# Kernel tuning notes

Hardware: AMD Instinct MI355X
Metric: run time of the kernel (lower is better)

The kernel has to match this reference:

```python
import jax, jax.numpy as jnp
import numpy as np

B, N, L, D, H, NLAYERS, V = 8, 1024, 16, 256, 4, 2, 32000
DH = D // H  # per-head dim


def setup_inputs() -> dict:
    key = jax.random.key(0)
    ks = jax.random.split(key, 7)
    cfg_adj = jax.random.randint(ks[0], (B, N, N), 0, 2, dtype=jnp.int32)
    cfg_nodes = jax.random.randint(ks[1], (B, N, L), 0, V, dtype=jnp.int32)
    cfg_len = jax.random.randint(ks[2], (B,), 1, N + 1, dtype=jnp.int32)
    emb = jax.random.normal(ks[3], (V, D), jnp.float32) * 0.02
    # xavier-ish scale for per-head projections and attention vectors
    W = jax.random.normal(ks[4], (NLAYERS, H, D, DH), jnp.float32) * np.float32(np.sqrt(2.0 / (D + DH)))
    a_src = jax.random.normal(ks[5], (NLAYERS, H, DH), jnp.float32) * 0.1
    a_dst = jax.random.normal(ks[6], (NLAYERS, H, DH), jnp.float32) * 0.1
    ln_scale = jnp.ones((NLAYERS, D), jnp.float32)
    ln_bias = jnp.zeros((NLAYERS, D), jnp.float32)
    return {"cfg_adj": cfg_adj, "cfg_nodes": cfg_nodes, "cfg_len": cfg_len,
            "emb": emb, "W": W, "a_src": a_src, "a_dst": a_dst,
            "ln_scale": ln_scale, "ln_bias": ln_bias}


def _layer_norm(x, scale, bias, eps=1e-5):
    mu = jnp.mean(x, axis=-1, keepdims=True)
    var = jnp.var(x, axis=-1, keepdims=True)
    return (x - mu) * jax.lax.rsqrt(var + eps) * scale + bias


def reference(cfg_adj, cfg_nodes, cfg_len, emb, W, a_src, a_dst, ln_scale, ln_bias):
    # node features: mean over token embeddings (dropout is identity in eval)
    node_feat = emb[cfg_nodes].mean(axis=2)                       # (B,N,D)
    # add self-loops once (repeated add+clamp in the original is idempotent)
    adj = jnp.minimum(cfg_adj + jnp.eye(N, dtype=cfg_adj.dtype)[None], 1)
    neg_mask = (adj == 0)[:, None]                                # (B,1,N,N)
    h = node_feat
    for l in range(NLAYERS):
        Wh = jnp.einsum('bnd,hdk->bhnk', h, W[l])                 # (B,H,N,DH)
        src = jnp.einsum('bhnk,hk->bhn', Wh, a_src[l])            # (B,H,N)
        dst = jnp.einsum('bhnk,hk->bhn', Wh, a_dst[l])            # (B,H,N)
        e = jax.nn.leaky_relu(src[:, :, :, None] + dst[:, :, None, :], 0.2)
        e = jnp.where(neg_mask, jnp.float32(-1e9), e)             # masked fill
        alpha = jax.nn.softmax(e, axis=-1)                        # (B,H,N,N)
        h_prime = jnp.einsum('bhnm,bhmk->bhnk', alpha, Wh)        # (B,H,N,DH)
        h_cat = jnp.transpose(h_prime, (0, 2, 1, 3)).reshape(B, N, D)
        h = _layer_norm(h + h_cat, ln_scale[l], ln_bias[l])
    return h, cfg_len
```

## Files before the change

kernel.cpp:

```cpp
#include <hip/hip_runtime.h>
#include <math.h>

#define B 8
#define N 1024
#define L 16
#define D 256
#define H 4
#define DH 64
#define NLAYERS 2
#define V 32000

typedef __attribute__((ext_vector_type(8))) short short8;
typedef __attribute__((ext_vector_type(4))) float f32x4;

union U8 { uint4 u; short8 s; };

__device__ inline unsigned short f2bf(float x) {
    unsigned u = __float_as_uint(x);
    u = (u + 0x7fff + ((u >> 16) & 1)) >> 16;
    return (unsigned short)u;
}
__device__ inline float bf2f(unsigned short x) {
    return __uint_as_float(((unsigned)x) << 16);
}


#define PACK_BLK 2048
#define WT_BLK   (NLAYERS * H * 4)
#define PRE_GRID (PACK_BLK + WT_BLK + 1)

__global__ __launch_bounds__(256) void k_pre(const int* __restrict__ adj,
                                             const float* __restrict__ W,
                                             const int* __restrict__ len,
                                             unsigned long long* __restrict__ pack,
                                             unsigned short* __restrict__ WT_sw,
                                             float* __restrict__ out_len) {
    int bid = blockIdx.x;
    int t = threadIdx.x;
    if (bid < PACK_BLK) {
        int row = bid * 4 + (t >> 6);
        int lane = t & 63;
        int n = row & (N - 1);
        const int* arow = adj + (long)row * N;
        unsigned long long* prow = pack + (size_t)row * 16;
        int g16 = lane & 15;
#pragma unroll
        for (int it = 0; it < 4; ++it) {
            int m0 = it * 256 + lane * 4;
            int4 a = *(const int4*)(arow + m0);
            unsigned nib = (unsigned)((a.x != 0) || (m0 == n))
                         | ((unsigned)((a.y != 0) || (m0 + 1 == n)) << 1)
                         | ((unsigned)((a.z != 0) || (m0 + 2 == n)) << 2)
                         | ((unsigned)((a.w != 0) || (m0 + 3 == n)) << 3);
            unsigned long long v = (unsigned long long)nib << (g16 * 4);
            v |= __shfl_xor(v, 1, 64);
            v |= __shfl_xor(v, 2, 64);
            v |= __shfl_xor(v, 4, 64);
            v |= __shfl_xor(v, 8, 64);
            if (g16 == 0) prow[it * 4 + (lane >> 4)] = v;
        }
    } else if (bid < PACK_BLK + WT_BLK) {
        int idx = bid - PACK_BLK;
        int lh = idx >> 2, q = idx & 3;
        const float* Wl = W + (size_t)lh * D * DH;
        int dh = t & 63;
        int d0 = q * 64 + (t >> 6) * 16;
#pragma unroll
        for (int i = 0; i < 16; ++i) {
            int d = d0 + i;
            WT_sw[(((size_t)lh * 8 + (d >> 5)) * 64 + dh) * 32 + (d & 31)] = f2bf(Wl[(size_t)d * DH + dh]);
        }
    } else {
        if (t < B) out_len[t] = (float)len[t];
    }
}

__device__ inline void wh_tile(const unsigned short* __restrict__ hA,
                               const unsigned short* __restrict__ WT_l,
                               const float* __restrict__ asrc_l,
                               const float* __restrict__ adst_l,
                               unsigned short* __restrict__ WhT_out,
                               float* __restrict__ srcv_out,
                               float* __restrict__ dstv_out,
                               int b, int n0, int hh, int lane) {
    int rowLane = lane & 15, quad = lane >> 4;
    int bh = b * H + hh;
    const unsigned short* abase = hA + rowLane * 32 + quad * 8;
    const unsigned short* bbase = WT_l + (size_t)hh * 16384 + rowLane * 32 + quad * 8;
    f32x4 acc[4] = {};
#pragma unroll
    for (int kc = 0; kc < 8; ++kc) {
        short8 af = *(const short8*)(abase + kc * 512);
#pragma unroll
        for (int c = 0; c < 4; ++c) {
            short8 bf = *(const short8*)(bbase + (size_t)kc * 2048 + c * 512);
            acc[c] = __builtin_amdgcn_mfma_f32_16x16x32_bf16(af, bf, acc[c], 0, 0, 0);
        }
    }
    int m0 = n0 + quad * 4;
    float ps[4] = {0.f, 0.f, 0.f, 0.f}, pd[4] = {0.f, 0.f, 0.f, 0.f};
#pragma unroll
    for (int c = 0; c < 4; ++c) {
        int dh = c * 16 + rowLane;
        ushort4 o;
        o.x = f2bf(acc[c][0]); o.y = f2bf(acc[c][1]);
        o.z = f2bf(acc[c][2]); o.w = f2bf(acc[c][3]);
        *(ushort4*)&WhT_out[(((size_t)bh * 32 + (m0 >> 5)) * 64 + dh) * 32 + (m0 & 31)] = o;
        float as = asrc_l[hh * DH + dh];
        float ad = adst_l[hh * DH + dh];
#pragma unroll
        for (int r = 0; r < 4; ++r) { ps[r] += acc[c][r] * as; pd[r] += acc[c][r] * ad; }
    }
#pragma unroll
    for (int off = 1; off < 16; off <<= 1) {
#pragma unroll
        for (int r = 0; r < 4; ++r) {
            ps[r] += __shfl_xor(ps[r], off, 64);
            pd[r] += __shfl_xor(pd[r], off, 64);
        }
    }
    if (rowLane == 0) {
#pragma unroll
        for (int r = 0; r < 4; ++r) {
            srcv_out[bh * N + m0 + r] = ps[r];
            dstv_out[bh * N + m0 + r] = pd[r];
        }
    }
}

__global__ __launch_bounds__(1024) void k_feat(const float* __restrict__ emb,
                                               const int* __restrict__ nodes,
                                               unsigned short* __restrict__ h_sw,
                                               const unsigned short* __restrict__ WT0,
                                               const float* __restrict__ asrc0,
                                               const float* __restrict__ adst0,
                                               unsigned short* __restrict__ WhT0,
                                               float* __restrict__ srcv0,
                                               float* __restrict__ dstv0) {
    __shared__ __align__(16) int nodesLds[256];
    __shared__ __align__(16) unsigned short hA[8 * 16 * 32];
    int tid = threadIdx.x;
    int bt = blockIdx.x;
    int b = bt >> 6, nt = bt & 63, n0 = nt * 16;
    if (tid < 256) nodesLds[tid] = nodes[(size_t)(b * N + n0) * L + tid];
    __syncthreads();
    int w = tid >> 6, lane = tid & 63;
    int d4 = lane * 4;
    const int* np = nodesLds + w * L;
    float4 s = make_float4(0.f, 0.f, 0.f, 0.f);
#pragma unroll
    for (int l = 0; l < L; ++l) {
        float4 v = *(const float4*)&emb[(size_t)np[l] * D + d4];
        s.x += v.x; s.y += v.y; s.z += v.z; s.w += v.w;
    }
    s.x *= (1.0f / L); s.y *= (1.0f / L); s.z *= (1.0f / L); s.w *= (1.0f / L);
    ushort4 o;
    o.x = f2bf(s.x); o.y = f2bf(s.y); o.z = f2bf(s.z); o.w = f2bf(s.w);
    int off = (d4 >> 5) * 512 + w * 32 + (d4 & 31);
    *(ushort4*)&hA[off] = o;
    *(ushort4*)&h_sw[((size_t)(b * 64 + nt) * 8) * 512 + off] = o;
    __syncthreads();
    if (w < 4) wh_tile(hA, WT0, asrc0, adst0, WhT0, srcv0, dstv0, b, n0, w, lane);
}

template <int FINAL>
__global__ __launch_bounds__(256) void k_attn_f(const unsigned long long* __restrict__ pack,
                                                const float* __restrict__ srcv_in,
                                                const float* __restrict__ dstv_in,
                                                const unsigned short* __restrict__ WhT_in,
                                                unsigned short* __restrict__ h_sw,
                                                const float* __restrict__ scale_l,
                                                const float* __restrict__ bias_l,
                                                const unsigned short* __restrict__ WT_next,
                                                const float* __restrict__ asrc_n,
                                                const float* __restrict__ adst_n,
                                                unsigned short* __restrict__ WhT_out,
                                                float* __restrict__ srcv_out,
                                                float* __restrict__ dstv_out,
                                                float* __restrict__ out) {
    __shared__ __align__(16) char smem[25600];
    float* dsts = (float*)smem;
    unsigned long long* packs = (unsigned long long*)(smem + 16384);
    float* xt = (float*)smem;
    unsigned short* hA = (unsigned short*)(smem + 17408);

    int tid = threadIdx.x;
    int bt = blockIdx.x;
    int b = bt >> 6, nt = bt & 63, n0 = nt * 16;
    int w = tid >> 6, lane = tid & 63;
    int rowLane = lane & 15, quad = lane >> 4;
    int bh = b * H + w;

    {
        const float* dv = dstv_in + (size_t)bh * N;
#pragma unroll
        for (int k = 0; k < 4; ++k)
            *(float4*)(dsts + w * 1024 + k * 256 + lane * 4) = *(const float4*)(dv + k * 256 + lane * 4);
        packs[tid] = pack[((size_t)(b * N + n0 + (tid >> 4))) * 16 + (tid & 15)];
    }
    __syncthreads();

    float src = srcv_in[bh * N + n0 + rowLane];
    float mx = src > 0.f ? src : 0.2f * src;
    const unsigned* prow = (const unsigned*)packs + rowLane * 32;
    const unsigned short* wbase = WhT_in + (size_t)bh * 65536 + rowLane * 32 + quad * 8;
    const float* dw = dsts + w * 1024 + quad * 8;

    f32x4 acc[4] = {};
    float sum0 = 0.f, sum1 = 0.f;
    short8 fb[2][4];
#pragma unroll
    for (int c = 0; c < 4; ++c) fb[0][c] = *(const short8*)(wbase + c * 512);
#pragma unroll 2
    for (int t2 = 0; t2 < 32; ++t2) {
        int cb = t2 & 1;
        int t2n = (t2 + 1) & 31;
#pragma unroll
        for (int c = 0; c < 4; ++c)
            fb[cb ^ 1][c] = *(const short8*)(wbase + (size_t)t2n * 2048 + c * 512);
        unsigned bits = (prow[t2] >> (quad * 8)) & 0xffu;
        float4 d0 = *(const float4*)(dw + t2 * 32);
        float4 d1 = *(const float4*)(dw + t2 * 32 + 4);
        float dd[8] = {d0.x, d0.y, d0.z, d0.w, d1.x, d1.y, d1.z, d1.w};
        unsigned pk[4];
#pragma unroll
        for (int j2 = 0; j2 < 4; ++j2) {
            float ea = src + dd[2 * j2];
            float eb = src + dd[2 * j2 + 1];
            ea = ea > 0.f ? ea : 0.2f * ea;
            eb = eb > 0.f ? eb : 0.2f * eb;
            float pa = ((bits >> (2 * j2)) & 1) ? __expf(ea - mx) : 0.f;
            float pb = ((bits >> (2 * j2 + 1)) & 1) ? __expf(eb - mx) : 0.f;
            sum0 += pa; sum1 += pb;
            pk[j2] = (__float_as_uint(pb) & 0xffff0000u) | (__float_as_uint(pa) >> 16);
        }
        U8 u; u.u = make_uint4(pk[0], pk[1], pk[2], pk[3]);
        short8 af = u.s;
        acc[0] = __builtin_amdgcn_mfma_f32_16x16x32_bf16(af, fb[cb][0], acc[0], 0, 0, 0);
        acc[1] = __builtin_amdgcn_mfma_f32_16x16x32_bf16(af, fb[cb][1], acc[1], 0, 0, 0);
        acc[2] = __builtin_amdgcn_mfma_f32_16x16x32_bf16(af, fb[cb][2], acc[2], 0, 0, 0);
        acc[3] = __builtin_amdgcn_mfma_f32_16x16x32_bf16(af, fb[cb][3], acc[3], 0, 0, 0);
    }
    float sum = sum0 + sum1;
    sum += __shfl_xor(sum, 16, 64);
    sum += __shfl_xor(sum, 32, 64);
    float inv[4];
#pragma unroll
    for (int r = 0; r < 4; ++r) inv[r] = 1.0f / __shfl(sum, quad * 4 + r, 64);

    __syncthreads();
#pragma unroll
    for (int c = 0; c < 4; ++c)
#pragma unroll
        for (int r = 0; r < 4; ++r)
            xt[(quad * 4 + r) * 268 + w * 64 + c * 16 + rowLane] = acc[c][r] * inv[r];
    __syncthreads();

    int row = tid >> 4, g = tid & 15;
    size_t hsb = ((size_t)(b * 64 + nt) * 8 + (g >> 1)) * 512 + row * 32 + (g & 1) * 16;
    U8 r0, r1;
    r0.u = *(const uint4*)(h_sw + hsb);
    r1.u = *(const uint4*)(h_sw + hsb + 8);
    float4 xr[4];
#pragma unroll
    for (int k = 0; k < 4; ++k) xr[k] = *(const float4*)(xt + row * 268 + g * 16 + k * 4);
    float xv[16];
    float s = 0.f, s2 = 0.f;
#pragma unroll
    for (int j = 0; j < 16; ++j) {
        unsigned short hv = (j < 8) ? ((const unsigned short*)&r0)[j] : ((const unsigned short*)&r1)[j - 8];
        float x = bf2f(hv) + ((const float*)xr)[j];
        xv[j] = x; s += x; s2 += x * x;
    }
#pragma unroll
    for (int off = 1; off < 16; off <<= 1) {
        s += __shfl_xor(s, off, 64);
        s2 += __shfl_xor(s2, off, 64);
    }
    float mu = s * (1.0f / D);
    float var = s2 * (1.0f / D) - mu * mu;
    float rstd = rsqrtf(var + 1e-5f);
    int d0 = g * 16;
    if (FINAL) {
        float* orow = out + ((size_t)(b * N) + n0 + row) * D + d0;
#pragma unroll
        for (int k = 0; k < 4; ++k) {
            float4 sc = *(const float4*)(scale_l + d0 + k * 4);
            float4 bi = *(const float4*)(bias_l + d0 + k * 4);
            float4 y;
            y.x = (xv[k * 4 + 0] - mu) * rstd * sc.x + bi.x;
            y.y = (xv[k * 4 + 1] - mu) * rstd * sc.y + bi.y;
            y.z = (xv[k * 4 + 2] - mu) * rstd * sc.z + bi.z;
            y.w = (xv[k * 4 + 3] - mu) * rstd * sc.w + bi.w;
            *(float4*)(orow + k * 4) = y;
        }
    } else {
        U8 o0, o1;
#pragma unroll
        for (int j = 0; j < 16; ++j) {
            float scv = scale_l[d0 + j];
            float biv = bias_l[d0 + j];
            unsigned short yb = f2bf((xv[j] - mu) * rstd * scv + biv);
            if (j < 8) ((unsigned short*)&o0)[j] = yb;
            else ((unsigned short*)&o1)[j - 8] = yb;
        }
        *(uint4*)(h_sw + hsb) = o0.u;
        *(uint4*)(h_sw + hsb + 8) = o1.u;
        unsigned short* ha = hA + (g >> 1) * 512 + row * 32 + (g & 1) * 16;
        *(uint4*)ha = o0.u;
        *(uint4*)(ha + 8) = o1.u;
        __syncthreads();
        wh_tile(hA, WT_next, asrc_n, adst_n, WhT_out, srcv_out, dstv_out, b, n0, w, lane);
    }
}

extern "C" void kernel_launch(void* const* d_in, const int* in_sizes, int n_in,
                              void* d_out, int out_size, void* d_ws, size_t ws_size,
                              hipStream_t stream) {
    const int* cfg_adj = (const int*)d_in[0];
    const int* cfg_nodes = (const int*)d_in[1];
    const int* cfg_len = (const int*)d_in[2];
    const float* emb = (const float*)d_in[3];
    const float* W = (const float*)d_in[4];
    const float* a_src = (const float*)d_in[5];
    const float* a_dst = (const float*)d_in[6];
    const float* ln_scale = (const float*)d_in[7];
    const float* ln_bias = (const float*)d_in[8];
    float* out = (float*)d_out;
    float* ws = (float*)d_ws;

    float* srcv0 = ws;
    float* dstv0 = srcv0 + (size_t)B * H * N;
    float* srcv1 = dstv0 + (size_t)B * H * N;
    float* dstv1 = srcv1 + (size_t)B * H * N;
    unsigned short* h_sw = (unsigned short*)(dstv1 + (size_t)B * H * N);
    unsigned short* WhT0 = h_sw + (size_t)B * N * D;
    unsigned short* WhT1 = WhT0 + (size_t)B * H * DH * N;
    unsigned short* WT_sw = WhT1 + (size_t)B * H * DH * N;
    unsigned long long* pack = (unsigned long long*)(WT_sw + (size_t)NLAYERS * H * DH * D);

    k_pre<<<PRE_GRID, 256, 0, stream>>>(cfg_adj, W, cfg_len, pack, WT_sw, out + (size_t)B * N * D);
    k_feat<<<B * 64, 1024, 0, stream>>>(emb, cfg_nodes, h_sw, WT_sw, a_src, a_dst,
                                        WhT0, srcv0, dstv0);
    k_attn_f<0><<<B * 64, 256, 0, stream>>>(pack, srcv0, dstv0, WhT0, h_sw,
                                            ln_scale, ln_bias,
                                            WT_sw + (size_t)H * DH * D,
                                            a_src + (size_t)H * DH, a_dst + (size_t)H * DH,
                                            WhT1, srcv1, dstv1, nullptr);
    k_attn_f<1><<<B * 64, 256, 0, stream>>>(pack, srcv1, dstv1, WhT1, h_sw,
                                            ln_scale + D, ln_bias + D,
                                            nullptr, nullptr, nullptr,
                                            nullptr, nullptr, nullptr, out);
}
```

Baseline: 173.5 us.

## Fuse all stages into one cooperative persistent kernel with grid syncs

Replaces the four separate launches (preprocess, feature, two attention layers) with one cooperative kernel of 256 blocks of 512 threads, using grid.sync between phases. Each block handles 32 nodes, keeps its adjacency bitmask and layer activations resident in LDS across phases, and no longer writes or reads the h_sw and pack buffers in global memory. This removes launch gaps and global round trips. In exchange the grid is smaller (256 blocks versus 512 or 2048), which lowers parallelism for the adjacency-packing and attention phases, and the grid barriers add their own cost.

```diff
diff --git a/kernel.cpp b/kernel.cpp
--- a/kernel.cpp
+++ b/kernel.cpp
@@ -1,5 +1,8 @@
 #include <hip/hip_runtime.h>
+#include <hip/hip_cooperative_groups.h>
 #include <math.h>
+
+namespace cg = cooperative_groups;
 
 #define B 8
 #define N 1024
@@ -24,68 +27,21 @@
     return __uint_as_float(((unsigned)x) << 16);
 }
 
-
-#define PACK_BLK 2048
-#define WT_BLK   (NLAYERS * H * 4)
-#define PRE_GRID (PACK_BLK + WT_BLK + 1)
-
-__global__ __launch_bounds__(256) void k_pre(const int* __restrict__ adj,
-                                             const float* __restrict__ W,
-                                             const int* __restrict__ len,
-                                             unsigned long long* __restrict__ pack,
-                                             unsigned short* __restrict__ WT_sw,
-                                             float* __restrict__ out_len) {
-    int bid = blockIdx.x;
-    int t = threadIdx.x;
-    if (bid < PACK_BLK) {
-        int row = bid * 4 + (t >> 6);
-        int lane = t & 63;
-        int n = row & (N - 1);
-        const int* arow = adj + (long)row * N;
-        unsigned long long* prow = pack + (size_t)row * 16;
-        int g16 = lane & 15;
-#pragma unroll
-        for (int it = 0; it < 4; ++it) {
-            int m0 = it * 256 + lane * 4;
-            int4 a = *(const int4*)(arow + m0);
-            unsigned nib = (unsigned)((a.x != 0) || (m0 == n))
-                         | ((unsigned)((a.y != 0) || (m0 + 1 == n)) << 1)
-                         | ((unsigned)((a.z != 0) || (m0 + 2 == n)) << 2)
-                         | ((unsigned)((a.w != 0) || (m0 + 3 == n)) << 3);
-            unsigned long long v = (unsigned long long)nib << (g16 * 4);
-            v |= __shfl_xor(v, 1, 64);
-            v |= __shfl_xor(v, 2, 64);
-            v |= __shfl_xor(v, 4, 64);
-            v |= __shfl_xor(v, 8, 64);
-            if (g16 == 0) prow[it * 4 + (lane >> 4)] = v;
-        }
-    } else if (bid < PACK_BLK + WT_BLK) {
-        int idx = bid - PACK_BLK;
-        int lh = idx >> 2, q = idx & 3;
-        const float* Wl = W + (size_t)lh * D * DH;
-        int dh = t & 63;
-        int d0 = q * 64 + (t >> 6) * 16;
-#pragma unroll
-        for (int i = 0; i < 16; ++i) {
-            int d = d0 + i;
-            WT_sw[(((size_t)lh * 8 + (d >> 5)) * 64 + dh) * 32 + (d & 31)] = f2bf(Wl[(size_t)d * DH + dh]);
-        }
-    } else {
-        if (t < B) out_len[t] = (float)len[t];
-    }
-}
-
-__device__ inline void wh_tile(const unsigned short* __restrict__ hA,
+#define SM_PACK 34304
+#define SM_HA   38400
+#define SM_SIZE 54784
+
+__device__ inline void wh_tile(const unsigned short* hA_t,
                                const unsigned short* __restrict__ WT_l,
                                const float* __restrict__ asrc_l,
                                const float* __restrict__ adst_l,
                                unsigned short* __restrict__ WhT_out,
                                float* __restrict__ srcv_out,
                                float* __restrict__ dstv_out,
-                               int b, int n0, int hh, int lane) {
+                               int b, int n0t, int hh, int lane) {
     int rowLane = lane & 15, quad = lane >> 4;
     int bh = b * H + hh;
-    const unsigned short* abase = hA + rowLane * 32 + quad * 8;
+    const unsigned short* abase = hA_t + rowLane * 32 + quad * 8;
     const unsigned short* bbase = WT_l + (size_t)hh * 16384 + rowLane * 32 + quad * 8;
     f32x4 acc[4] = {};
 #pragma unroll
@@ -97,7 +53,7 @@
             acc[c] = __builtin_amdgcn_mfma_f32_16x16x32_bf16(af, bf, acc[c], 0, 0, 0);
         }
     }
-    int m0 = n0 + quad * 4;
+    int m0 = n0t + quad * 4;
     float ps[4] = {0.f, 0.f, 0.f, 0.f}, pd[4] = {0.f, 0.f, 0.f, 0.f};
 #pragma unroll
     for (int c = 0; c < 4; ++c) {
@@ -128,83 +84,45 @@
     }
 }
 
-__global__ __launch_bounds__(1024) void k_feat(const float* __restrict__ emb,
-                                               const int* __restrict__ nodes,
-                                               unsigned short* __restrict__ h_sw,
-                                               const unsigned short* __restrict__ WT0,
-                                               const float* __restrict__ asrc0,
-                                               const float* __restrict__ adst0,
-                                               unsigned short* __restrict__ WhT0,
-                                               float* __restrict__ srcv0,
-                                               float* __restrict__ dstv0) {
-    __shared__ __align__(16) int nodesLds[256];
-    __shared__ __align__(16) unsigned short hA[8 * 16 * 32];
-    int tid = threadIdx.x;
-    int bt = blockIdx.x;
-    int b = bt >> 6, nt = bt & 63, n0 = nt * 16;
-    if (tid < 256) nodesLds[tid] = nodes[(size_t)(b * N + n0) * L + tid];
+template <int FINAL>
+__device__ inline void attn_phase(char* smem,
+                                  const float* __restrict__ srcv_in,
+                                  const float* __restrict__ dstv_in,
+                                  const unsigned short* __restrict__ WhT_in,
+                                  const float* __restrict__ scale_l,
+                                  const float* __restrict__ bias_l,
+                                  const unsigned short* __restrict__ WT_next,
+                                  const float* __restrict__ asrc_n,
+                                  const float* __restrict__ adst_n,
+                                  unsigned short* __restrict__ WhT_out,
+                                  float* __restrict__ srcv_out,
+                                  float* __restrict__ dstv_out,
+                                  float* __restrict__ out,
+                                  int b, int n0base, int tid) {
+    float* dsts = (float*)smem;
+    const unsigned long long* packs = (const unsigned long long*)(smem + SM_PACK);
+    unsigned short* hAall = (unsigned short*)(smem + SM_HA);
+
+    int wg = tid >> 6, lane = tid & 63;
+    int tg = wg >> 2, hh = wg & 3;
+    int rowLane = lane & 15, quad = lane >> 4;
+    int bh = b * H + hh;
+    int n0t = n0base + tg * 16;
+
+    {
+        const float* dv = dstv_in + (size_t)bh * N + tg * 512;
+#pragma unroll
+        for (int k = 0; k < 2; ++k)
+            *(float4*)(dsts + hh * 1024 + tg * 512 + k * 256 + lane * 4) =
+                *(const float4*)(dv + k * 256 + lane * 4);
+    }
     __syncthreads();
-    int w = tid >> 6, lane = tid & 63;
-    int d4 = lane * 4;
-    const int* np = nodesLds + w * L;
-    float4 s = make_float4(0.f, 0.f, 0.f, 0.f);
-#pragma unroll
-    for (int l = 0; l < L; ++l) {
-        float4 v = *(const float4*)&emb[(size_t)np[l] * D + d4];
-        s.x += v.x; s.y += v.y; s.z += v.z; s.w += v.w;
-    }
-    s.x *= (1.0f / L); s.y *= (1.0f / L); s.z *= (1.0f / L); s.w *= (1.0f / L);
-    ushort4 o;
-    o.x = f2bf(s.x); o.y = f2bf(s.y); o.z = f2bf(s.z); o.w = f2bf(s.w);
-    int off = (d4 >> 5) * 512 + w * 32 + (d4 & 31);
-    *(ushort4*)&hA[off] = o;
-    *(ushort4*)&h_sw[((size_t)(b * 64 + nt) * 8) * 512 + off] = o;
-    __syncthreads();
-    if (w < 4) wh_tile(hA, WT0, asrc0, adst0, WhT0, srcv0, dstv0, b, n0, w, lane);
-}
-
-template <int FINAL>
-__global__ __launch_bounds__(256) void k_attn_f(const unsigned long long* __restrict__ pack,
-                                                const float* __restrict__ srcv_in,
-                                                const float* __restrict__ dstv_in,
-                                                const unsigned short* __restrict__ WhT_in,
-                                                unsigned short* __restrict__ h_sw,
-                                                const float* __restrict__ scale_l,
-                                                const float* __restrict__ bias_l,
-                                                const unsigned short* __restrict__ WT_next,
-                                                const float* __restrict__ asrc_n,
-                                                const float* __restrict__ adst_n,
-                                                unsigned short* __restrict__ WhT_out,
-                                                float* __restrict__ srcv_out,
-                                                float* __restrict__ dstv_out,
-                                                float* __restrict__ out) {
-    __shared__ __align__(16) char smem[25600];
-    float* dsts = (float*)smem;
-    unsigned long long* packs = (unsigned long long*)(smem + 16384);
-    float* xt = (float*)smem;
-    unsigned short* hA = (unsigned short*)(smem + 17408);
-
-    int tid = threadIdx.x;
-    int bt = blockIdx.x;
-    int b = bt >> 6, nt = bt & 63, n0 = nt * 16;
-    int w = tid >> 6, lane = tid & 63;
-    int rowLane = lane & 15, quad = lane >> 4;
-    int bh = b * H + w;
-
-    {
-        const float* dv = dstv_in + (size_t)bh * N;
-#pragma unroll
-        for (int k = 0; k < 4; ++k)
-            *(float4*)(dsts + w * 1024 + k * 256 + lane * 4) = *(const float4*)(dv + k * 256 + lane * 4);
-        packs[tid] = pack[((size_t)(b * N + n0 + (tid >> 4))) * 16 + (tid & 15)];
-    }
-    __syncthreads();
-
-    float src = srcv_in[bh * N + n0 + rowLane];
+
+    float src = srcv_in[bh * N + n0t + rowLane];
     float mx = src > 0.f ? src : 0.2f * src;
-    const unsigned* prow = (const unsigned*)packs + rowLane * 32;
+    const unsigned* prow = (const unsigned*)packs + (tg * 16 + rowLane) * 32;
     const unsigned short* wbase = WhT_in + (size_t)bh * 65536 + rowLane * 32 + quad * 8;
-    const float* dw = dsts + w * 1024 + quad * 8;
+    const float* dw = dsts + hh * 1024 + quad * 8;
 
     f32x4 acc[4] = {};
     float sum0 = 0.f, sum1 = 0.f;
@@ -249,21 +167,24 @@
     for (int r = 0; r < 4; ++r) inv[r] = 1.0f / __shfl(sum, quad * 4 + r, 64);
 
     __syncthreads();
+    float* xt = (float*)smem + tg * 4288;
 #pragma unroll
     for (int c = 0; c < 4; ++c)
 #pragma unroll
         for (int r = 0; r < 4; ++r)
-            xt[(quad * 4 + r) * 268 + w * 64 + c * 16 + rowLane] = acc[c][r] * inv[r];
+            xt[(quad * 4 + r) * 268 + hh * 64 + c * 16 + rowLane] = acc[c][r] * inv[r];
     __syncthreads();
 
-    int row = tid >> 4, g = tid & 15;
-    size_t hsb = ((size_t)(b * 64 + nt) * 8 + (g >> 1)) * 512 + row * 32 + (g & 1) * 16;
+    int t8 = tid >> 8, rowg = tid & 255;
+    int row = rowg >> 4, g = rowg & 15;
+    const float* xtt = (float*)smem + t8 * 4288;
+    unsigned short* ha = hAall + t8 * 4096 + (g >> 1) * 512 + row * 32 + (g & 1) * 16;
     U8 r0, r1;
-    r0.u = *(const uint4*)(h_sw + hsb);
-    r1.u = *(const uint4*)(h_sw + hsb + 8);
+    r0.u = *(const uint4*)ha;
+    r1.u = *(const uint4*)(ha + 8);
     float4 xr[4];
 #pragma unroll
-    for (int k = 0; k < 4; ++k) xr[k] = *(const float4*)(xt + row * 268 + g * 16 + k * 4);
+    for (int k = 0; k < 4; ++k) xr[k] = *(const float4*)(xtt + row * 268 + g * 16 + k * 4);
     float xv[16];
     float s = 0.f, s2 = 0.f;
 #pragma unroll
@@ -282,7 +203,7 @@
     float rstd = rsqrtf(var + 1e-5f);
     int d0 = g * 16;
     if (FINAL) {
-        float* orow = out + ((size_t)(b * N) + n0 + row) * D + d0;
+        float* orow = out + ((size_t)(b * N) + n0base + t8 * 16 + row) * D + d0;
 #pragma unroll
         for (int k = 0; k < 4; ++k) {
             float4 sc = *(const float4*)(scale_l + d0 + k * 4);
@@ -304,14 +225,107 @@
             if (j < 8) ((unsigned short*)&o0)[j] = yb;
             else ((unsigned short*)&o1)[j - 8] = yb;
         }
-        *(uint4*)(h_sw + hsb) = o0.u;
-        *(uint4*)(h_sw + hsb + 8) = o1.u;
-        unsigned short* ha = hA + (g >> 1) * 512 + row * 32 + (g & 1) * 16;
         *(uint4*)ha = o0.u;
         *(uint4*)(ha + 8) = o1.u;
         __syncthreads();
-        wh_tile(hA, WT_next, asrc_n, adst_n, WhT_out, srcv_out, dstv_out, b, n0, w, lane);
-    }
+        wh_tile(hAall + tg * 4096, WT_next, asrc_n, adst_n, WhT_out, srcv_out, dstv_out,
+                b, n0t, hh, lane);
+    }
+}
+
+__global__ __launch_bounds__(512, 2) void k_mega(
+    const int* __restrict__ adj, const float* __restrict__ W,
+    const int* __restrict__ len, const float* __restrict__ emb,
+    const int* __restrict__ nodes,
+    const float* __restrict__ a_src, const float* __restrict__ a_dst,
+    const float* __restrict__ ln_scale, const float* __restrict__ ln_bias,
+    float* __restrict__ out,
+    unsigned short* __restrict__ WT_sw,
+    unsigned short* __restrict__ WhT0, unsigned short* __restrict__ WhT1,
+    float* __restrict__ srcv0, float* __restrict__ dstv0,
+    float* __restrict__ srcv1, float* __restrict__ dstv1) {
+    __shared__ __align__(16) char smem[SM_SIZE];
+    int* nodesLds = (int*)smem;
+    unsigned long long* packs = (unsigned long long*)(smem + SM_PACK);
+    unsigned short* hAall = (unsigned short*)(smem + SM_HA);
+
+    cg::grid_group grid = cg::this_grid();
+    int tid = threadIdx.x;
+    int bt = blockIdx.x;
+    int b = bt >> 5, ntPair = bt & 31, n0base = ntPair * 32;
+    int wg = tid >> 6, lane = tid & 63;
+    int tg = wg >> 2, hh = wg & 3;
+
+    nodesLds[tid] = nodes[((size_t)(b * N + n0base)) * L + tid];
+    __syncthreads();
+    {
+        int d4 = lane * 4;
+#pragma unroll
+        for (int r = 0; r < 4; ++r) {
+            int r16 = wg * 4 + r;
+            const int* np = nodesLds + r16 * L;
+            float4 s = make_float4(0.f, 0.f, 0.f, 0.f);
+#pragma unroll
+            for (int l = 0; l < L; ++l) {
+                float4 v = *(const float4*)&emb[(size_t)np[l] * D + d4];
+                s.x += v.x; s.y += v.y; s.z += v.z; s.w += v.w;
+            }
+            ushort4 o;
+            o.x = f2bf(s.x * (1.0f / L)); o.y = f2bf(s.y * (1.0f / L));
+            o.z = f2bf(s.z * (1.0f / L)); o.w = f2bf(s.w * (1.0f / L));
+            *(ushort4*)&hAall[(r16 >> 4) * 4096 + (d4 >> 5) * 512 + (r16 & 15) * 32 + (d4 & 31)] = o;
+        }
+    }
+    {
+        int g16 = lane & 15;
+#pragma unroll
+        for (int r = 0; r < 4; ++r) {
+            int r16 = wg * 4 + r;
+            int n = n0base + r16;
+            const int* arow = adj + ((size_t)(b * N + n)) * N;
+#pragma unroll
+            for (int it = 0; it < 4; ++it) {
+                int m0 = it * 256 + lane * 4;
+                int4 a = *(const int4*)(arow + m0);
+                unsigned nib = (unsigned)((a.x != 0) || (m0 == n))
+                             | ((unsigned)((a.y != 0) || (m0 + 1 == n)) << 1)
+                             | ((unsigned)((a.z != 0) || (m0 + 2 == n)) << 2)
+                             | ((unsigned)((a.w != 0) || (m0 + 3 == n)) << 3);
+                unsigned long long v = (unsigned long long)nib << (g16 * 4);
+                v |= __shfl_xor(v, 1, 64);
+                v |= __shfl_xor(v, 2, 64);
+                v |= __shfl_xor(v, 4, 64);
+                v |= __shfl_xor(v, 8, 64);
+                if (g16 == 0) packs[r16 * 16 + it * 4 + (lane >> 4)] = v;
+            }
+        }
+    }
+    if (bt < NLAYERS * H * 4) {
+        int lh = bt >> 2, q = bt & 3;
+        const float* Wl = W + (size_t)lh * D * DH;
+        int dh = tid & 63;
+        int d0 = q * 64 + (tid >> 6) * 8;
+#pragma unroll
+        for (int i = 0; i < 8; ++i) {
+            int d = d0 + i;
+            WT_sw[(((size_t)lh * 8 + (d >> 5)) * 64 + dh) * 32 + (d & 31)] = f2bf(Wl[(size_t)d * DH + dh]);
+        }
+    }
+    if (bt == 32 && tid < B) out[(size_t)B * N * D + tid] = (float)len[tid];
+
+    grid.sync();
+    wh_tile(hAall + tg * 4096, WT_sw, a_src, a_dst, WhT0, srcv0, dstv0,
+            b, n0base + tg * 16, hh, lane);
+    grid.sync();
+    attn_phase<0>(smem, srcv0, dstv0, WhT0,
+                  ln_scale, ln_bias,
+                  WT_sw + (size_t)H * 16384, a_src + (size_t)H * DH, a_dst + (size_t)H * DH,
+                  WhT1, srcv1, dstv1, nullptr, b, n0base, tid);
+    grid.sync();
+    attn_phase<1>(smem, srcv1, dstv1, WhT1,
+                  ln_scale + D, ln_bias + D,
+                  nullptr, nullptr, nullptr,
+                  nullptr, nullptr, nullptr, out, b, n0base, tid);
 }
 
 extern "C" void kernel_launch(void* const* d_in, const int* in_sizes, int n_in,
@@ -333,22 +347,14 @@
     float* dstv0 = srcv0 + (size_t)B * H * N;
     float* srcv1 = dstv0 + (size_t)B * H * N;
     float* dstv1 = srcv1 + (size_t)B * H * N;
-    unsigned short* h_sw = (unsigned short*)(dstv1 + (size_t)B * H * N);
-    unsigned short* WhT0 = h_sw + (size_t)B * N * D;
+    unsigned short* WhT0 = (unsigned short*)(dstv1 + (size_t)B * H * N);
     unsigned short* WhT1 = WhT0 + (size_t)B * H * DH * N;
     unsigned short* WT_sw = WhT1 + (size_t)B * H * DH * N;
-    unsigned long long* pack = (unsigned long long*)(WT_sw + (size_t)NLAYERS * H * DH * D);
-
-    k_pre<<<PRE_GRID, 256, 0, stream>>>(cfg_adj, W, cfg_len, pack, WT_sw, out + (size_t)B * N * D);
-    k_feat<<<B * 64, 1024, 0, stream>>>(emb, cfg_nodes, h_sw, WT_sw, a_src, a_dst,
-                                        WhT0, srcv0, dstv0);
-    k_attn_f<0><<<B * 64, 256, 0, stream>>>(pack, srcv0, dstv0, WhT0, h_sw,
-                                            ln_scale, ln_bias,
-                                            WT_sw + (size_t)H * DH * D,
-                                            a_src + (size_t)H * DH, a_dst + (size_t)H * DH,
-                                            WhT1, srcv1, dstv1, nullptr);
-    k_attn_f<1><<<B * 64, 256, 0, stream>>>(pack, srcv1, dstv1, WhT1, h_sw,
-                                            ln_scale + D, ln_bias + D,
-                                            nullptr, nullptr, nullptr,
-                                            nullptr, nullptr, nullptr, out);
-}
+
+    void* args[] = {(void*)&cfg_adj, (void*)&W, (void*)&cfg_len, (void*)&emb,
+                    (void*)&cfg_nodes, (void*)&a_src, (void*)&a_dst,
+                    (void*)&ln_scale, (void*)&ln_bias, (void*)&out,
+                    (void*)&WT_sw, (void*)&WhT0, (void*)&WhT1,
+                    (void*)&srcv0, (void*)&dstv0, (void*)&srcv1, (void*)&dstv1};
+    hipLaunchCooperativeKernel((void*)k_mega, dim3(B * 32), dim3(512), args, 0, stream);
+}
```

Result: slower. 289.2 us (+66.7%).

## Fuse adjacency packing, weight transpose and layer-0 projection into one kernel

Applied to the files above, without the earlier changes.

Merges the preprocessing kernel (adjacency bit-packing, weight transpose/convert) and the feature/layer-0 projection kernel into a single 256-thread launch. Each block gathers embeddings for its 16 nodes, packs the matching 16 adjacency rows, and computes layer-0 Wh straight from fp32 W converted to bf16 in registers. Only layer-1 weights are still pre-transposed, by extra blocks. This removes one launch and the global round trip for layer-0 weights, at the cost of redundant per-block W conversion, high register pressure from a 32-fragment B array, and a longer serial chain per block.

```diff
diff --git a/kernel.cpp b/kernel.cpp
--- a/kernel.cpp
+++ b/kernel.cpp
@@ -25,67 +25,165 @@
 }
 
 
-#define PACK_BLK 2048
-#define WT_BLK   (NLAYERS * H * 4)
-#define PRE_GRID (PACK_BLK + WT_BLK + 1)
-
-__global__ __launch_bounds__(256) void k_pre(const int* __restrict__ adj,
-                                             const float* __restrict__ W,
-                                             const int* __restrict__ len,
-                                             unsigned long long* __restrict__ pack,
-                                             unsigned short* __restrict__ WT_sw,
-                                             float* __restrict__ out_len) {
-    int bid = blockIdx.x;
-    int t = threadIdx.x;
-    if (bid < PACK_BLK) {
-        int row = bid * 4 + (t >> 6);
-        int lane = t & 63;
-        int n = row & (N - 1);
-        const int* arow = adj + (long)row * N;
-        unsigned long long* prow = pack + (size_t)row * 16;
-        int g16 = lane & 15;
-#pragma unroll
-        for (int it = 0; it < 4; ++it) {
-            int m0 = it * 256 + lane * 4;
-            int4 a = *(const int4*)(arow + m0);
-            unsigned nib = (unsigned)((a.x != 0) || (m0 == n))
-                         | ((unsigned)((a.y != 0) || (m0 + 1 == n)) << 1)
-                         | ((unsigned)((a.z != 0) || (m0 + 2 == n)) << 2)
-                         | ((unsigned)((a.w != 0) || (m0 + 3 == n)) << 3);
-            unsigned long long v = (unsigned long long)nib << (g16 * 4);
-            v |= __shfl_xor(v, 1, 64);
-            v |= __shfl_xor(v, 2, 64);
-            v |= __shfl_xor(v, 4, 64);
-            v |= __shfl_xor(v, 8, 64);
-            if (g16 == 0) prow[it * 4 + (lane >> 4)] = v;
-        }
-    } else if (bid < PACK_BLK + WT_BLK) {
-        int idx = bid - PACK_BLK;
-        int lh = idx >> 2, q = idx & 3;
-        const float* Wl = W + (size_t)lh * D * DH;
-        int dh = t & 63;
-        int d0 = q * 64 + (t >> 6) * 16;
+__global__ __launch_bounds__(256) void k_fpw(
+    const float* __restrict__ emb, const int* __restrict__ nodes,
+    const int* __restrict__ adj, const int* __restrict__ len,
+    const float* __restrict__ W,
+    const float* __restrict__ a_src, const float* __restrict__ a_dst,
+    unsigned short* __restrict__ h_sw, unsigned long long* __restrict__ pack,
+    unsigned short* __restrict__ WT_sw,
+    unsigned short* __restrict__ WhT0, float* __restrict__ srcv0, float* __restrict__ dstv0,
+    float* __restrict__ out_len) {
+    int bt = blockIdx.x, tid = threadIdx.x;
+    if (bt >= 512) {
+        int idx = bt - 512;
+        int hh = idx >> 2, q = idx & 3;
+        const float* Wl = W + (size_t)(H + hh) * D * DH;
+        int dh = tid & 63;
+        int d0 = q * 64 + (tid >> 6) * 16;
 #pragma unroll
         for (int i = 0; i < 16; ++i) {
             int d = d0 + i;
-            WT_sw[(((size_t)lh * 8 + (d >> 5)) * 64 + dh) * 32 + (d & 31)] = f2bf(Wl[(size_t)d * DH + dh]);
-        }
-    } else {
-        if (t < B) out_len[t] = (float)len[t];
-    }
-}
-
-__device__ inline void wh_tile(const unsigned short* __restrict__ hA,
+            WT_sw[(((size_t)hh * 8 + (d >> 5)) * 64 + dh) * 32 + (d & 31)] = f2bf(Wl[(size_t)d * DH + dh]);
+        }
+        return;
+    }
+    __shared__ __align__(16) int nodesLds[256];
+    __shared__ __align__(16) unsigned short hA[4096];
+    int b = bt >> 6, nt = bt & 63, n0 = nt * 16;
+    if (bt == 0 && tid < B) out_len[tid] = (float)len[tid];
+    nodesLds[tid] = nodes[((size_t)(b * N + n0)) * L + tid];
+    __syncthreads();
+
+    {
+        int row = tid >> 4, cg = tid & 15;
+        const int* np = nodesLds + row * L;
+        float4 a0 = make_float4(0.f, 0.f, 0.f, 0.f), a1 = a0, a2 = a0, a3 = a0;
+#pragma unroll
+        for (int l = 0; l < L; ++l) {
+            const float* e = emb + (size_t)np[l] * D + cg * 16;
+            float4 v0 = *(const float4*)(e);
+            float4 v1 = *(const float4*)(e + 4);
+            float4 v2 = *(const float4*)(e + 8);
+            float4 v3 = *(const float4*)(e + 12);
+            a0.x += v0.x; a0.y += v0.y; a0.z += v0.z; a0.w += v0.w;
+            a1.x += v1.x; a1.y += v1.y; a1.z += v1.z; a1.w += v1.w;
+            a2.x += v2.x; a2.y += v2.y; a2.z += v2.z; a2.w += v2.w;
+            a3.x += v3.x; a3.y += v3.y; a3.z += v3.z; a3.w += v3.w;
+        }
+        const float sc = 1.0f / L;
+        U8 o0, o1;
+        float f0[8] = {a0.x, a0.y, a0.z, a0.w, a1.x, a1.y, a1.z, a1.w};
+        float f1[8] = {a2.x, a2.y, a2.z, a2.w, a3.x, a3.y, a3.z, a3.w};
+#pragma unroll
+        for (int j = 0; j < 8; ++j) {
+            ((unsigned short*)&o0)[j] = f2bf(f0[j] * sc);
+            ((unsigned short*)&o1)[j] = f2bf(f1[j] * sc);
+        }
+        size_t lbase = ((size_t)(cg >> 1)) * 512 + row * 32 + (cg & 1) * 16;
+        *(uint4*)&hA[lbase] = o0.u;
+        *(uint4*)&hA[lbase + 8] = o1.u;
+        size_t gbase = ((size_t)(b * 64 + nt)) * 4096 + lbase;
+        *(uint4*)&h_sw[gbase] = o0.u;
+        *(uint4*)&h_sw[gbase + 8] = o1.u;
+    }
+
+    {
+        int w = tid >> 6, lane = tid & 63, g16 = lane & 15;
+#pragma unroll
+        for (int r = 0; r < 4; ++r) {
+            int r16 = w * 4 + r;
+            int n = n0 + r16;
+            const int* arow = adj + ((size_t)(b * N + n)) * N;
+            unsigned long long* prow = pack + ((size_t)(b * N + n)) * 16;
+#pragma unroll
+            for (int it = 0; it < 4; ++it) {
+                int m0 = it * 256 + lane * 4;
+                int4 a = *(const int4*)(arow + m0);
+                unsigned nib = (unsigned)((a.x != 0) || (m0 == n))
+                             | ((unsigned)((a.y != 0) || (m0 + 1 == n)) << 1)
+                             | ((unsigned)((a.z != 0) || (m0 + 2 == n)) << 2)
+                             | ((unsigned)((a.w != 0) || (m0 + 3 == n)) << 3);
+                unsigned long long v = (unsigned long long)nib << (g16 * 4);
+                v |= __shfl_xor(v, 1, 64);
+                v |= __shfl_xor(v, 2, 64);
+                v |= __shfl_xor(v, 4, 64);
+                v |= __shfl_xor(v, 8, 64);
+                if (g16 == 0) prow[it * 4 + (lane >> 4)] = v;
+            }
+        }
+    }
+    __syncthreads();
+
+    {
+        int w = tid >> 6, lane = tid & 63;
+        int rowLane = lane & 15, quad = lane >> 4;
+        int bh = b * H + w;
+        const float* W0 = W + (size_t)w * D * DH;
+        const float* wb = W0 + (size_t)(quad * 8) * DH + rowLane;
+        short8 bfr[8][4];
+#pragma unroll
+        for (int kc = 0; kc < 8; ++kc)
+#pragma unroll
+            for (int c = 0; c < 4; ++c) {
+                short8 f;
+#pragma unroll
+                for (int j = 0; j < 8; ++j)
+                    f[j] = (short)f2bf(wb[(size_t)(kc * 32 + j) * DH + c * 16]);
+                bfr[kc][c] = f;
+            }
+        const unsigned short* abase = hA + rowLane * 32 + quad * 8;
+        f32x4 acc[4] = {};
+#pragma unroll
+        for (int kc = 0; kc < 8; ++kc) {
+            short8 af = *(const short8*)(abase + kc * 512);
+#pragma unroll
+            for (int c = 0; c < 4; ++c)
+                acc[c] = __builtin_amdgcn_mfma_f32_16x16x32_bf16(af, bfr[kc][c], acc[c], 0, 0, 0);
+        }
+        int m0 = n0 + quad * 4;
+        float ps[4] = {0.f, 0.f, 0.f, 0.f}, pd[4] = {0.f, 0.f, 0.f, 0.f};
+#pragma unroll
+        for (int c = 0; c < 4; ++c) {
+            int dh = c * 16 + rowLane;
+            ushort4 o;
+            o.x = f2bf(acc[c][0]); o.y = f2bf(acc[c][1]);
+            o.z = f2bf(acc[c][2]); o.w = f2bf(acc[c][3]);
+            *(ushort4*)&WhT0[(((size_t)bh * 32 + (m0 >> 5)) * 64 + dh) * 32 + (m0 & 31)] = o;
+            float as = a_src[w * DH + dh];
+            float ad = a_dst[w * DH + dh];
+#pragma unroll
+            for (int r = 0; r < 4; ++r) { ps[r] += acc[c][r] * as; pd[r] += acc[c][r] * ad; }
+        }
+#pragma unroll
+        for (int off = 1; off < 16; off <<= 1) {
+#pragma unroll
+            for (int r = 0; r < 4; ++r) {
+                ps[r] += __shfl_xor(ps[r], off, 64);
+                pd[r] += __shfl_xor(pd[r], off, 64);
+            }
+        }
+        if (rowLane == 0) {
+#pragma unroll
+            for (int r = 0; r < 4; ++r) {
+                srcv0[bh * N + m0 + r] = ps[r];
+                dstv0[bh * N + m0 + r] = pd[r];
+            }
+        }
+    }
+}
+
+__device__ inline void wh_tile(const unsigned short* hA_t,
                                const unsigned short* __restrict__ WT_l,
                                const float* __restrict__ asrc_l,
                                const float* __restrict__ adst_l,
                                unsigned short* __restrict__ WhT_out,
                                float* __restrict__ srcv_out,
                                float* __restrict__ dstv_out,
-                               int b, int n0, int hh, int lane) {
+                               int b, int n0t, int hh, int lane) {
     int rowLane = lane & 15, quad = lane >> 4;
     int bh = b * H + hh;
-    const unsigned short* abase = hA + rowLane * 32 + quad * 8;
+    const unsigned short* abase = hA_t + rowLane * 32 + quad * 8;
     const unsigned short* bbase = WT_l + (size_t)hh * 16384 + rowLane * 32 + quad * 8;
     f32x4 acc[4] = {};
 #pragma unroll
@@ -97,7 +195,7 @@
             acc[c] = __builtin_amdgcn_mfma_f32_16x16x32_bf16(af, bf, acc[c], 0, 0, 0);
         }
     }
-    int m0 = n0 + quad * 4;
+    int m0 = n0t + quad * 4;
     float ps[4] = {0.f, 0.f, 0.f, 0.f}, pd[4] = {0.f, 0.f, 0.f, 0.f};
 #pragma unroll
     for (int c = 0; c < 4; ++c) {
@@ -126,41 +224,6 @@
             dstv_out[bh * N + m0 + r] = pd[r];
         }
     }
-}
-
-__global__ __launch_bounds__(1024) void k_feat(const float* __restrict__ emb,
-                                               const int* __restrict__ nodes,
-                                               unsigned short* __restrict__ h_sw,
-                                               const unsigned short* __restrict__ WT0,
-                                               const float* __restrict__ asrc0,
-                                               const float* __restrict__ adst0,
-                                               unsigned short* __restrict__ WhT0,
-                                               float* __restrict__ srcv0,
-                                               float* __restrict__ dstv0) {
-    __shared__ __align__(16) int nodesLds[256];
-    __shared__ __align__(16) unsigned short hA[8 * 16 * 32];
-    int tid = threadIdx.x;
-    int bt = blockIdx.x;
-    int b = bt >> 6, nt = bt & 63, n0 = nt * 16;
-    if (tid < 256) nodesLds[tid] = nodes[(size_t)(b * N + n0) * L + tid];
-    __syncthreads();
-    int w = tid >> 6, lane = tid & 63;
-    int d4 = lane * 4;
-    const int* np = nodesLds + w * L;
-    float4 s = make_float4(0.f, 0.f, 0.f, 0.f);
-#pragma unroll
-    for (int l = 0; l < L; ++l) {
-        float4 v = *(const float4*)&emb[(size_t)np[l] * D + d4];
-        s.x += v.x; s.y += v.y; s.z += v.z; s.w += v.w;
-    }
-    s.x *= (1.0f / L); s.y *= (1.0f / L); s.z *= (1.0f / L); s.w *= (1.0f / L);
-    ushort4 o;
-    o.x = f2bf(s.x); o.y = f2bf(s.y); o.z = f2bf(s.z); o.w = f2bf(s.w);
-    int off = (d4 >> 5) * 512 + w * 32 + (d4 & 31);
-    *(ushort4*)&hA[off] = o;
-    *(ushort4*)&h_sw[((size_t)(b * 64 + nt) * 8) * 512 + off] = o;
-    __syncthreads();
-    if (w < 4) wh_tile(hA, WT0, asrc0, adst0, WhT0, srcv0, dstv0, b, n0, w, lane);
 }
 
 template <int FINAL>
@@ -337,14 +400,14 @@
     unsigned short* WhT0 = h_sw + (size_t)B * N * D;
     unsigned short* WhT1 = WhT0 + (size_t)B * H * DH * N;
     unsigned short* WT_sw = WhT1 + (size_t)B * H * DH * N;
-    unsigned long long* pack = (unsigned long long*)(WT_sw + (size_t)NLAYERS * H * DH * D);
-
-    k_pre<<<PRE_GRID, 256, 0, stream>>>(cfg_adj, W, cfg_len, pack, WT_sw, out + (size_t)B * N * D);
-    k_feat<<<B * 64, 1024, 0, stream>>>(emb, cfg_nodes, h_sw, WT_sw, a_src, a_dst,
-                                        WhT0, srcv0, dstv0);
+    unsigned long long* pack = (unsigned long long*)(WT_sw + (size_t)H * D * DH);
+
+    k_fpw<<<512 + 16, 256, 0, stream>>>(emb, cfg_nodes, cfg_adj, cfg_len, W,
+                                        a_src, a_dst, h_sw, pack, WT_sw,
+                                        WhT0, srcv0, dstv0, out + (size_t)B * N * D);
     k_attn_f<0><<<B * 64, 256, 0, stream>>>(pack, srcv0, dstv0, WhT0, h_sw,
                                             ln_scale, ln_bias,
-                                            WT_sw + (size_t)H * DH * D,
+                                            WT_sw,
                                             a_src + (size_t)H * DH, a_dst + (size_t)H * DH,
                                             WhT1, srcv1, dstv1, nullptr);
     k_attn_f<1><<<B * 64, 256, 0, stream>>>(pack, srcv1, dstv1, WhT1, h_sw,
```

Result: slower. 209.6 us (+20.8%).
